# Kernel tuning notes

Hardware: AMD Instinct MI355X
Metric: run time of the kernel (lower is better)

## Reference

```python
import jax, jax.numpy as jnp
import numpy as np

N_NODES = 100000


def _graph_conv_right(feat, src, dst, W, b, n_nodes):
    # DGL GraphConv(norm='right'): since in_feats > out_feats, apply weight first,
    # then sum-aggregate messages over edges, divide by in-degree (clamped >= 1),
    # add bias, then relu activation.
    h = feat @ W                                   # [N, out]
    msg = jnp.take(h, src, axis=0)                 # [E, out] gather from source nodes
    agg = jax.ops.segment_sum(msg, dst, num_segments=n_nodes)  # [N, out]
    deg = jax.ops.segment_sum(jnp.ones_like(dst, dtype=feat.dtype), dst,
                              num_segments=n_nodes)
    deg = jnp.clip(deg, 1.0, None)                 # allow_zero_in_degree
    out = agg / deg[:, None] + b
    return jax.nn.relu(out)


def setup_inputs() -> dict:
    key = jax.random.key(0)
    ks = jax.random.split(key, 6)
    n_edges = 3200000
    in_dim, hidden_dim, out_dim = 128, 32, 12
    features = jax.random.normal(ks[0], (N_NODES, in_dim), dtype=jnp.float32)
    src = jax.random.randint(ks[1], (n_edges,), 0, N_NODES, dtype=jnp.int64 if jax.config.jax_enable_x64 else jnp.int32)
    dst = jax.random.randint(ks[2], (n_edges,), 0, N_NODES, dtype=jnp.int64 if jax.config.jax_enable_x64 else jnp.int32)
    W1 = jax.random.normal(ks[3], (in_dim, hidden_dim), dtype=jnp.float32) * (1.0 / np.sqrt(in_dim))
    b1 = jnp.zeros((hidden_dim,), dtype=jnp.float32)
    W2 = jax.random.normal(ks[4], (hidden_dim, out_dim), dtype=jnp.float32) * (1.0 / np.sqrt(hidden_dim))
    b2 = jnp.zeros((out_dim,), dtype=jnp.float32)
    return {"features": features, "src": src, "dst": dst,
            "W1": W1, "b1": b1, "W2": W2, "b2": b2}


def reference(features, src, dst, W1, b1, W2, b2):
    x = _graph_conv_right(features, src, dst, W1, b1, N_NODES)
    x = jax.nn.relu(x)  # extra F.relu after layer1 (idempotent, kept for fidelity)
    x = _graph_conv_right(x, src, dst, W2, b2, N_NODES)
    return x
```

## Files before the change

kernel.cpp:

```cpp
#include <hip/hip_runtime.h>
#include <hip/hip_fp16.h>

#define N_IN   128
#define HID    32
#define ODIM   12
#define RNODES 128
#define NBMAX  800
#define NBK2   1024
#define BCAP   4608
#define CHUNK  4096

__global__ __launch_bounds__(256) void gemm1_kernel(const float* __restrict__ feat,
                                                    const float* __restrict__ W1,
                                                    __half* __restrict__ h1, int nNodes) {
    __shared__ float sF[64 * 132];
    __shared__ float sW[N_IN * HID];
    const int tid = threadIdx.x;
    const int nb  = blockIdx.x * 64;

    {
        const float4* Wv  = (const float4*)W1;
        float4*       sWv = (float4*)sW;
        #pragma unroll
        for (int i = 0; i < 4; ++i) sWv[tid + 256 * i] = Wv[tid + 256 * i];
    }
    #pragma unroll
    for (int i = 0; i < 8; ++i) {
        int f   = tid + 256 * i;
        int row = f >> 5;
        int c4  = f & 31;
        int n   = nb + row;
        float4 v = make_float4(0.f, 0.f, 0.f, 0.f);
        if (n < nNodes) v = *(const float4*)(feat + (size_t)n * N_IN + c4 * 4);
        *(float4*)(sF + row * 132 + c4 * 4) = v;
    }
    __syncthreads();

    const int og = tid & 7;
    const int ng = tid >> 3;
    const int o0 = og * 4;
    const float* f0 = sF + ng * 132;
    const float* f1 = sF + (ng + 32) * 132;

    float acc0[4] = {0.f, 0.f, 0.f, 0.f};
    float acc1[4] = {0.f, 0.f, 0.f, 0.f};
    #pragma unroll 8
    for (int k = 0; k < N_IN; k += 4) {
        float4 a0 = *(const float4*)(f0 + k);
        float4 a1 = *(const float4*)(f1 + k);
        const float a0v[4] = {a0.x, a0.y, a0.z, a0.w};
        const float a1v[4] = {a1.x, a1.y, a1.z, a1.w};
        #pragma unroll
        for (int j = 0; j < 4; ++j) {
            float4 w = *(const float4*)(sW + (k + j) * HID + o0);
            acc0[0] += a0v[j] * w.x; acc0[1] += a0v[j] * w.y;
            acc0[2] += a0v[j] * w.z; acc0[3] += a0v[j] * w.w;
            acc1[0] += a1v[j] * w.x; acc1[1] += a1v[j] * w.y;
            acc1[2] += a1v[j] * w.z; acc1[3] += a1v[j] * w.w;
        }
    }
    int n0 = nb + ng, n1 = nb + ng + 32;
    if (n0 < nNodes) {
        union { __half2 h[2]; float2 f; } u;
        u.h[0] = __floats2half2_rn(acc0[0], acc0[1]);
        u.h[1] = __floats2half2_rn(acc0[2], acc0[3]);
        *(float2*)(h1 + (size_t)n0 * HID + o0) = u.f;
    }
    if (n1 < nNodes) {
        union { __half2 h[2]; float2 f; } u;
        u.h[0] = __floats2half2_rn(acc1[0], acc1[1]);
        u.h[1] = __floats2half2_rn(acc1[2], acc1[3]);
        *(float2*)(h1 + (size_t)n1 * HID + o0) = u.f;
    }
}

__global__ __launch_bounds__(512) void bplace_kernel(const int* __restrict__ src,
                                                     const int* __restrict__ dst,
                                                     int* __restrict__ bcur,
                                                     int* __restrict__ pairs, int nEdges) {
    __shared__ int      lh[NBK2];
    __shared__ int      lcur[NBK2];
    __shared__ int      gofs[NBK2];
    __shared__ int      sAux[512];
    __shared__ int      lst[CHUNK];
    __shared__ unsigned short lbk[CHUNK];

    const int tid  = threadIdx.x;
    const int base = blockIdx.x * CHUNK;
    const int m    = min(CHUNK, nEdges - base);

    lh[tid] = 0; lh[tid + 512] = 0;
    __syncthreads();

    int4 dv[2], sv[2];
    bool ok[2];
    #pragma unroll
    for (int k = 0; k < 2; ++k) {
        int e = base + k * 2048 + tid * 4;
        ok[k] = (e < nEdges);
        if (ok[k]) {
            dv[k] = *(const int4*)(dst + e);
            sv[k] = *(const int4*)(src + e);
        }
    }
    #pragma unroll
    for (int k = 0; k < 2; ++k) {
        if (ok[k]) {
            atomicAdd(&lh[dv[k].x >> 7], 1);
            atomicAdd(&lh[dv[k].y >> 7], 1);
            atomicAdd(&lh[dv[k].z >> 7], 1);
            atomicAdd(&lh[dv[k].w >> 7], 1);
        }
    }
    __syncthreads();

    int c0 = lh[2 * tid], c1 = lh[2 * tid + 1];
    int tsum = c0 + c1;
    sAux[tid] = tsum;
    __syncthreads();
    int inc = tsum;
    for (int off = 1; off < 512; off <<= 1) {
        int t = (tid >= off) ? sAux[tid - off] : 0;
        __syncthreads();
        inc += t;
        sAux[tid] = inc;
        __syncthreads();
    }
    int excl = inc - tsum;
    lh[2 * tid]     = excl;
    lh[2 * tid + 1] = excl + c0;
    lcur[2 * tid]     = excl;
    lcur[2 * tid + 1] = excl + c0;
    gofs[2 * tid]     = (c0 > 0) ? atomicAdd(&bcur[2 * tid], c0) : 0;
    gofs[2 * tid + 1] = (c1 > 0) ? atomicAdd(&bcur[2 * tid + 1], c1) : 0;
    __syncthreads();

    #pragma unroll
    for (int k = 0; k < 2; ++k) {
        if (ok[k]) {
            int b, p;
            b = dv[k].x >> 7; p = atomicAdd(&lcur[b], 1); lst[p] = ((dv[k].x & 127) << 17) | sv[k].x; lbk[p] = (unsigned short)b;
            b = dv[k].y >> 7; p = atomicAdd(&lcur[b], 1); lst[p] = ((dv[k].y & 127) << 17) | sv[k].y; lbk[p] = (unsigned short)b;
            b = dv[k].z >> 7; p = atomicAdd(&lcur[b], 1); lst[p] = ((dv[k].z & 127) << 17) | sv[k].z; lbk[p] = (unsigned short)b;
            b = dv[k].w >> 7; p = atomicAdd(&lcur[b], 1); lst[p] = ((dv[k].w & 127) << 17) | sv[k].w; lbk[p] = (unsigned short)b;
        }
    }
    __syncthreads();

    for (int i = tid; i < m; i += 512) {
        int b = lbk[i];
        int cap = gofs[b] + (i - lh[b]);
        if (cap < (b + 1) * BCAP - (b * BCAP) + 0) {}
        int rank = gofs[b] + (i - lh[b]);
        if (rank < BCAP) pairs[(size_t)b * BCAP + rank] = lst[i];
    }
}

__global__ __launch_bounds__(512) void agg1_kernel(const __half* __restrict__ h1,
                                                   const int* __restrict__ bcur,
                                                   const int* __restrict__ pairs,
                                                   const float* __restrict__ b1,
                                                   const float* __restrict__ W2,
                                                   __half* __restrict__ h2,
                                                   float* __restrict__ rdeg, int nNodes) {
    __shared__ int   sorted[BCAP];
    __shared__ int   hist[RNODES];
    __shared__ int   scn[RNODES];
    __shared__ int   cur[RNODES];
    __shared__ float sW2[HID * ODIM];
    const int tid = threadIdx.x;
    const int bkt = blockIdx.x;
    const int cnt = min(bcur[bkt], BCAP);
    const size_t pb = (size_t)bkt * BCAP;

    if (tid < RNODES) hist[tid] = 0;
    if (tid < 96) ((float4*)sW2)[tid] = ((const float4*)W2)[tid];
    __syncthreads();

    for (int i = tid; i < cnt; i += 512) atomicAdd(&hist[pairs[pb + i] >> 17], 1);
    __syncthreads();

    int v0 = (tid < RNODES) ? hist[tid] : 0;
    if (tid < RNODES) scn[tid] = v0;
    __syncthreads();
    int inc = v0;
    for (int off = 1; off < RNODES; off <<= 1) {
        int t = (tid < RNODES && tid >= off) ? scn[tid - off] : 0;
        __syncthreads();
        if (tid < RNODES) { inc += t; scn[tid] = inc; }
        __syncthreads();
    }
    if (tid < RNODES) { scn[tid] = inc - v0; cur[tid] = inc - v0; }
    __syncthreads();

    for (int i = tid; i < cnt; i += 512) {
        int v = pairs[pb + i];
        int pos = atomicAdd(&cur[v >> 17], 1);
        sorted[pos] = v & 0x1FFFF;
    }
    __syncthreads();

    const int c   = tid & 15;
    const int grp = tid >> 4;
    const __half2* h1v = (const __half2*)h1;
    const int col = (c < ODIM) ? c : 0;

    #pragma unroll
    for (int g = 0; g < 4; ++g) {
        int nl = g * 32 + grp;
        int n  = bkt * RNODES + nl;
        if (n >= nNodes) continue;
        int dcnt = hist[nl];
        int beg  = scn[nl];
        int end  = beg + dcnt;

        float2 s0 = {0.f, 0.f}, s1 = {0.f, 0.f}, s2 = {0.f, 0.f}, s3 = {0.f, 0.f};
        int i = beg;
        for (; i + 4 <= end; i += 4) {
            int e0 = sorted[i], e1 = sorted[i + 1], e2 = sorted[i + 2], e3 = sorted[i + 3];
            float2 f0 = __half22float2(h1v[(size_t)e0 * 16 + c]);
            float2 f1 = __half22float2(h1v[(size_t)e1 * 16 + c]);
            float2 f2 = __half22float2(h1v[(size_t)e2 * 16 + c]);
            float2 f3 = __half22float2(h1v[(size_t)e3 * 16 + c]);
            s0.x += f0.x; s0.y += f0.y;
            s1.x += f1.x; s1.y += f1.y;
            s2.x += f2.x; s2.y += f2.y;
            s3.x += f3.x; s3.y += f3.y;
        }
        for (; i < end; ++i) {
            float2 f = __half22float2(h1v[(size_t)sorted[i] * 16 + c]);
            s0.x += f.x; s0.y += f.y;
        }
        float sumx = (s0.x + s1.x) + (s2.x + s3.x);
        float sumy = (s0.y + s1.y) + (s2.y + s3.y);

        float rd = 1.f / (float)(dcnt < 1 ? 1 : dcnt);
        float x0 = sumx * rd + b1[2 * c];
        float x1 = sumy * rd + b1[2 * c + 1];
        x0 = x0 > 0.f ? x0 : 0.f;
        x1 = x1 > 0.f ? x1 : 0.f;

        float acc = 0.f;
        #pragma unroll
        for (int k = 0; k < 16; ++k) {
            float xk0 = __shfl(x0, k, 16);
            float xk1 = __shfl(x1, k, 16);
            acc += xk0 * sW2[(2 * k) * ODIM + col] + xk1 * sW2[(2 * k + 1) * ODIM + col];
        }
        if (c < ODIM) h2[(size_t)n * ODIM + c] = __float2half(acc);
        if (c == 0)   rdeg[n] = rd;
    }
}

__global__ __launch_bounds__(512) void agg2_kernel(const __half* __restrict__ h2,
                                                   const int* __restrict__ bcur,
                                                   const int* __restrict__ pairs,
                                                   const float* __restrict__ rdeg,
                                                   const float* __restrict__ b2,
                                                   float* __restrict__ out, int nNodes) {
    __shared__ int sorted[BCAP];
    __shared__ int hist[RNODES];
    __shared__ int scn[RNODES];
    __shared__ int cur[RNODES];
    const int tid = threadIdx.x;
    const int bkt = blockIdx.x;
    const int cnt = min(bcur[bkt], BCAP);
    const size_t pb = (size_t)bkt * BCAP;

    if (tid < RNODES) hist[tid] = 0;
    __syncthreads();

    for (int i = tid; i < cnt; i += 512) atomicAdd(&hist[pairs[pb + i] >> 17], 1);
    __syncthreads();

    int v0 = (tid < RNODES) ? hist[tid] : 0;
    if (tid < RNODES) scn[tid] = v0;
    __syncthreads();
    int inc = v0;
    for (int off = 1; off < RNODES; off <<= 1) {
        int t = (tid < RNODES && tid >= off) ? scn[tid - off] : 0;
        __syncthreads();
        if (tid < RNODES) { inc += t; scn[tid] = inc; }
        __syncthreads();
    }
    if (tid < RNODES) { scn[tid] = inc - v0; cur[tid] = inc - v0; }
    __syncthreads();

    for (int i = tid; i < cnt; i += 512) {
        int v = pairs[pb + i];
        int pos = atomicAdd(&cur[v >> 17], 1);
        sorted[pos] = v & 0x1FFFF;
    }
    __syncthreads();

    const int c   = tid & 7;
    const int grp = tid >> 3;
    const int cc  = (c < 6) ? c : 0;
    const __half2* h2v = (const __half2*)h2;

    #pragma unroll
    for (int g = 0; g < 2; ++g) {
        int nl = g * 64 + grp;
        int n  = bkt * RNODES + nl;
        if (n >= nNodes) continue;
        int dcnt = hist[nl];
        int beg  = scn[nl];
        int end  = beg + dcnt;

        float2 s0 = {0.f, 0.f}, s1 = {0.f, 0.f}, s2 = {0.f, 0.f}, s3 = {0.f, 0.f};
        int i = beg;
        for (; i + 4 <= end; i += 4) {
            int e0 = sorted[i], e1 = sorted[i + 1], e2 = sorted[i + 2], e3 = sorted[i + 3];
            float2 f0 = __half22float2(h2v[(size_t)e0 * 6 + cc]);
            float2 f1 = __half22float2(h2v[(size_t)e1 * 6 + cc]);
            float2 f2 = __half22float2(h2v[(size_t)e2 * 6 + cc]);
            float2 f3 = __half22float2(h2v[(size_t)e3 * 6 + cc]);
            s0.x += f0.x; s0.y += f0.y;
            s1.x += f1.x; s1.y += f1.y;
            s2.x += f2.x; s2.y += f2.y;
            s3.x += f3.x; s3.y += f3.y;
        }
        for (; i < end; ++i) {
            float2 f = __half22float2(h2v[(size_t)sorted[i] * 6 + cc]);
            s0.x += f.x; s0.y += f.y;
        }
        float sumx = (s0.x + s1.x) + (s2.x + s3.x);
        float sumy = (s0.y + s1.y) + (s2.y + s3.y);

        float rd = rdeg[n];
        float w0 = sumx * rd + b2[2 * cc];
        float w1 = sumy * rd + b2[2 * cc + 1];
        w0 = w0 > 0.f ? w0 : 0.f;
        w1 = w1 > 0.f ? w1 : 0.f;
        if (c < 6) *(float2*)(out + (size_t)n * ODIM + 2 * c) = make_float2(w0, w1);
    }
}

extern "C" void kernel_launch(void* const* d_in, const int* in_sizes, int n_in,
                              void* d_out, int out_size, void* d_ws, size_t ws_size,
                              hipStream_t stream) {
    const float* feat = (const float*)d_in[0];
    const int*   src  = (const int*)d_in[1];
    const int*   dst  = (const int*)d_in[2];
    const float* W1   = (const float*)d_in[3];
    const float* b1   = (const float*)d_in[4];
    const float* W2   = (const float*)d_in[5];
    const float* b2   = (const float*)d_in[6];
    float* out = (float*)d_out;

    const int nEdges = in_sizes[1];
    const int nNodes = in_sizes[0] / N_IN;
    const int nb     = (nNodes + RNODES - 1) / RNODES;

    __half* h1   = (__half*)d_ws;
    __half* h2   = h1 + (size_t)nNodes * HID;
    float*  rdeg = (float*)(h2 + (size_t)nNodes * ODIM);
    int*    bcur = (int*)(rdeg + nNodes);
    int*    pairs = bcur + NBK2;

    hipMemsetAsync(bcur, 0, NBK2 * sizeof(int), stream);

    gemm1_kernel<<<(nNodes + 63) / 64, 256, 0, stream>>>(feat, W1, h1, nNodes);
    bplace_kernel<<<(nEdges + CHUNK - 1) / CHUNK, 512, 0, stream>>>(src, dst, bcur, pairs, nEdges);
    agg1_kernel<<<nb, 512, 0, stream>>>(h1, bcur, pairs, b1, W2, h2, rdeg, nNodes);
    agg2_kernel<<<nb, 512, 0, stream>>>(h2, bcur, pairs, rdeg, b2, out, nNodes);
}
```

Before: 238.9 us.

## Persist CSR from agg1 and simplify agg2 to direct row-range gathers

agg1 now writes its per-bucket sorted source indices back into the pairs buffer, along with a global row start and count for each node. agg2 no longer repeats the histogram, prefix scan and scatter sort; it reads this CSR directly with one 8-thread group per node in smaller 256-thread blocks. Both gather loops are also unrolled to 8 edges to keep more loads in flight. The cost is an extra global write of about 3.2M indices plus two per-node arrays in agg1, and agg2 reads the indices from global memory instead of LDS.

```diff
diff --git a/kernel.cpp b/kernel.cpp
--- a/kernel.cpp
+++ b/kernel.cpp
@@ -127,8 +127,8 @@
         __syncthreads();
     }
     int excl = inc - tsum;
-    lh[2 * tid]     = excl;
-    lh[2 * tid + 1] = excl + c0;
+    lh[2 * tid]       = excl;
+    lh[2 * tid + 1]   = excl + c0;
     lcur[2 * tid]     = excl;
     lcur[2 * tid + 1] = excl + c0;
     gofs[2 * tid]     = (c0 > 0) ? atomicAdd(&bcur[2 * tid], c0) : 0;
@@ -149,8 +149,6 @@
 
     for (int i = tid; i < m; i += 512) {
         int b = lbk[i];
-        int cap = gofs[b] + (i - lh[b]);
-        if (cap < (b + 1) * BCAP - (b * BCAP) + 0) {}
         int rank = gofs[b] + (i - lh[b]);
         if (rank < BCAP) pairs[(size_t)b * BCAP + rank] = lst[i];
     }
@@ -158,11 +156,13 @@
 
 __global__ __launch_bounds__(512) void agg1_kernel(const __half* __restrict__ h1,
                                                    const int* __restrict__ bcur,
-                                                   const int* __restrict__ pairs,
+                                                   int* __restrict__ pairs,
                                                    const float* __restrict__ b1,
                                                    const float* __restrict__ W2,
                                                    __half* __restrict__ h2,
-                                                   float* __restrict__ rdeg, int nNodes) {
+                                                   float* __restrict__ rdeg,
+                                                   int* __restrict__ rowstartg,
+                                                   int* __restrict__ countg, int nNodes) {
     __shared__ int   sorted[BCAP];
     __shared__ int   hist[RNODES];
     __shared__ int   scn[RNODES];
@@ -200,6 +200,15 @@
     }
     __syncthreads();
 
+    for (int i = tid; i < cnt; i += 512) pairs[pb + i] = sorted[i];
+    if (tid < RNODES) {
+        int n = bkt * RNODES + tid;
+        if (n < nNodes) {
+            rowstartg[n] = (int)pb + scn[tid];
+            countg[n]    = hist[tid];
+        }
+    }
+
     const int c   = tid & 15;
     const int grp = tid >> 4;
     const __half2* h1v = (const __half2*)h1;
@@ -216,16 +225,30 @@
 
         float2 s0 = {0.f, 0.f}, s1 = {0.f, 0.f}, s2 = {0.f, 0.f}, s3 = {0.f, 0.f};
         int i = beg;
+        for (; i + 8 <= end; i += 8) {
+            int e0 = sorted[i],     e1 = sorted[i + 1], e2 = sorted[i + 2], e3 = sorted[i + 3];
+            int e4 = sorted[i + 4], e5 = sorted[i + 5], e6 = sorted[i + 6], e7 = sorted[i + 7];
+            float2 f0 = __half22float2(h1v[(size_t)e0 * 16 + c]);
+            float2 f1 = __half22float2(h1v[(size_t)e1 * 16 + c]);
+            float2 f2 = __half22float2(h1v[(size_t)e2 * 16 + c]);
+            float2 f3 = __half22float2(h1v[(size_t)e3 * 16 + c]);
+            float2 f4 = __half22float2(h1v[(size_t)e4 * 16 + c]);
+            float2 f5 = __half22float2(h1v[(size_t)e5 * 16 + c]);
+            float2 f6 = __half22float2(h1v[(size_t)e6 * 16 + c]);
+            float2 f7 = __half22float2(h1v[(size_t)e7 * 16 + c]);
+            s0.x += f0.x; s0.y += f0.y;  s1.x += f1.x; s1.y += f1.y;
+            s2.x += f2.x; s2.y += f2.y;  s3.x += f3.x; s3.y += f3.y;
+            s0.x += f4.x; s0.y += f4.y;  s1.x += f5.x; s1.y += f5.y;
+            s2.x += f6.x; s2.y += f6.y;  s3.x += f7.x; s3.y += f7.y;
+        }
         for (; i + 4 <= end; i += 4) {
             int e0 = sorted[i], e1 = sorted[i + 1], e2 = sorted[i + 2], e3 = sorted[i + 3];
             float2 f0 = __half22float2(h1v[(size_t)e0 * 16 + c]);
             float2 f1 = __half22float2(h1v[(size_t)e1 * 16 + c]);
             float2 f2 = __half22float2(h1v[(size_t)e2 * 16 + c]);
             float2 f3 = __half22float2(h1v[(size_t)e3 * 16 + c]);
-            s0.x += f0.x; s0.y += f0.y;
-            s1.x += f1.x; s1.y += f1.y;
-            s2.x += f2.x; s2.y += f2.y;
-            s3.x += f3.x; s3.y += f3.y;
+            s0.x += f0.x; s0.y += f0.y;  s1.x += f1.x; s1.y += f1.y;
+            s2.x += f2.x; s2.y += f2.y;  s3.x += f3.x; s3.y += f3.y;
         }
         for (; i < end; ++i) {
             float2 f = __half22float2(h1v[(size_t)sorted[i] * 16 + c]);
@@ -252,88 +275,64 @@
     }
 }
 
-__global__ __launch_bounds__(512) void agg2_kernel(const __half* __restrict__ h2,
-                                                   const int* __restrict__ bcur,
-                                                   const int* __restrict__ pairs,
+__global__ __launch_bounds__(256) void agg2_kernel(const __half* __restrict__ h2,
+                                                   const int* __restrict__ rowstartg,
+                                                   const int* __restrict__ countg,
+                                                   const int* __restrict__ eidx,
                                                    const float* __restrict__ rdeg,
                                                    const float* __restrict__ b2,
                                                    float* __restrict__ out, int nNodes) {
-    __shared__ int sorted[BCAP];
-    __shared__ int hist[RNODES];
-    __shared__ int scn[RNODES];
-    __shared__ int cur[RNODES];
     const int tid = threadIdx.x;
-    const int bkt = blockIdx.x;
-    const int cnt = min(bcur[bkt], BCAP);
-    const size_t pb = (size_t)bkt * BCAP;
-
-    if (tid < RNODES) hist[tid] = 0;
-    __syncthreads();
-
-    for (int i = tid; i < cnt; i += 512) atomicAdd(&hist[pairs[pb + i] >> 17], 1);
-    __syncthreads();
-
-    int v0 = (tid < RNODES) ? hist[tid] : 0;
-    if (tid < RNODES) scn[tid] = v0;
-    __syncthreads();
-    int inc = v0;
-    for (int off = 1; off < RNODES; off <<= 1) {
-        int t = (tid < RNODES && tid >= off) ? scn[tid - off] : 0;
-        __syncthreads();
-        if (tid < RNODES) { inc += t; scn[tid] = inc; }
-        __syncthreads();
-    }
-    if (tid < RNODES) { scn[tid] = inc - v0; cur[tid] = inc - v0; }
-    __syncthreads();
-
-    for (int i = tid; i < cnt; i += 512) {
-        int v = pairs[pb + i];
-        int pos = atomicAdd(&cur[v >> 17], 1);
-        sorted[pos] = v & 0x1FFFF;
-    }
-    __syncthreads();
-
-    const int c   = tid & 7;
-    const int grp = tid >> 3;
+    const int n = blockIdx.x * 32 + (tid >> 3);
+    const int c = tid & 7;
+    if (n >= nNodes) return;
+
+    const int cnt = countg[n];
+    const int beg = rowstartg[n];
+    const int end = beg + cnt;
     const int cc  = (c < 6) ? c : 0;
     const __half2* h2v = (const __half2*)h2;
 
-    #pragma unroll
-    for (int g = 0; g < 2; ++g) {
-        int nl = g * 64 + grp;
-        int n  = bkt * RNODES + nl;
-        if (n >= nNodes) continue;
-        int dcnt = hist[nl];
-        int beg  = scn[nl];
-        int end  = beg + dcnt;
-
-        float2 s0 = {0.f, 0.f}, s1 = {0.f, 0.f}, s2 = {0.f, 0.f}, s3 = {0.f, 0.f};
-        int i = beg;
-        for (; i + 4 <= end; i += 4) {
-            int e0 = sorted[i], e1 = sorted[i + 1], e2 = sorted[i + 2], e3 = sorted[i + 3];
-            float2 f0 = __half22float2(h2v[(size_t)e0 * 6 + cc]);
-            float2 f1 = __half22float2(h2v[(size_t)e1 * 6 + cc]);
-            float2 f2 = __half22float2(h2v[(size_t)e2 * 6 + cc]);
-            float2 f3 = __half22float2(h2v[(size_t)e3 * 6 + cc]);
-            s0.x += f0.x; s0.y += f0.y;
-            s1.x += f1.x; s1.y += f1.y;
-            s2.x += f2.x; s2.y += f2.y;
-            s3.x += f3.x; s3.y += f3.y;
-        }
-        for (; i < end; ++i) {
-            float2 f = __half22float2(h2v[(size_t)sorted[i] * 6 + cc]);
-            s0.x += f.x; s0.y += f.y;
-        }
-        float sumx = (s0.x + s1.x) + (s2.x + s3.x);
-        float sumy = (s0.y + s1.y) + (s2.y + s3.y);
-
-        float rd = rdeg[n];
-        float w0 = sumx * rd + b2[2 * cc];
-        float w1 = sumy * rd + b2[2 * cc + 1];
-        w0 = w0 > 0.f ? w0 : 0.f;
-        w1 = w1 > 0.f ? w1 : 0.f;
-        if (c < 6) *(float2*)(out + (size_t)n * ODIM + 2 * c) = make_float2(w0, w1);
-    }
+    float2 s0 = {0.f, 0.f}, s1 = {0.f, 0.f}, s2 = {0.f, 0.f}, s3 = {0.f, 0.f};
+    int i = beg;
+    for (; i + 8 <= end; i += 8) {
+        int e0 = eidx[i],     e1 = eidx[i + 1], e2 = eidx[i + 2], e3 = eidx[i + 3];
+        int e4 = eidx[i + 4], e5 = eidx[i + 5], e6 = eidx[i + 6], e7 = eidx[i + 7];
+        float2 f0 = __half22float2(h2v[(size_t)e0 * 6 + cc]);
+        float2 f1 = __half22float2(h2v[(size_t)e1 * 6 + cc]);
+        float2 f2 = __half22float2(h2v[(size_t)e2 * 6 + cc]);
+        float2 f3 = __half22float2(h2v[(size_t)e3 * 6 + cc]);
+        float2 f4 = __half22float2(h2v[(size_t)e4 * 6 + cc]);
+        float2 f5 = __half22float2(h2v[(size_t)e5 * 6 + cc]);
+        float2 f6 = __half22float2(h2v[(size_t)e6 * 6 + cc]);
+        float2 f7 = __half22float2(h2v[(size_t)e7 * 6 + cc]);
+        s0.x += f0.x; s0.y += f0.y;  s1.x += f1.x; s1.y += f1.y;
+        s2.x += f2.x; s2.y += f2.y;  s3.x += f3.x; s3.y += f3.y;
+        s0.x += f4.x; s0.y += f4.y;  s1.x += f5.x; s1.y += f5.y;
+        s2.x += f6.x; s2.y += f6.y;  s3.x += f7.x; s3.y += f7.y;
+    }
+    for (; i + 4 <= end; i += 4) {
+        int e0 = eidx[i], e1 = eidx[i + 1], e2 = eidx[i + 2], e3 = eidx[i + 3];
+        float2 f0 = __half22float2(h2v[(size_t)e0 * 6 + cc]);
+        float2 f1 = __half22float2(h2v[(size_t)e1 * 6 + cc]);
+        float2 f2 = __half22float2(h2v[(size_t)e2 * 6 + cc]);
+        float2 f3 = __half22float2(h2v[(size_t)e3 * 6 + cc]);
+        s0.x += f0.x; s0.y += f0.y;  s1.x += f1.x; s1.y += f1.y;
+        s2.x += f2.x; s2.y += f2.y;  s3.x += f3.x; s3.y += f3.y;
+    }
+    for (; i < end; ++i) {
+        float2 f = __half22float2(h2v[(size_t)eidx[i] * 6 + cc]);
+        s0.x += f.x; s0.y += f.y;
+    }
+    float sumx = (s0.x + s1.x) + (s2.x + s3.x);
+    float sumy = (s0.y + s1.y) + (s2.y + s3.y);
+
+    float rd = rdeg[n];
+    float w0 = sumx * rd + b2[2 * cc];
+    float w1 = sumy * rd + b2[2 * cc + 1];
+    w0 = w0 > 0.f ? w0 : 0.f;
+    w1 = w1 > 0.f ? w1 : 0.f;
+    if (c < 6) *(float2*)(out + (size_t)n * ODIM + 2 * c) = make_float2(w0, w1);
 }
 
 extern "C" void kernel_launch(void* const* d_in, const int* in_sizes, int n_in,
@@ -352,16 +351,18 @@
     const int nNodes = in_sizes[0] / N_IN;
     const int nb     = (nNodes + RNODES - 1) / RNODES;
 
-    __half* h1   = (__half*)d_ws;
-    __half* h2   = h1 + (size_t)nNodes * HID;
-    float*  rdeg = (float*)(h2 + (size_t)nNodes * ODIM);
-    int*    bcur = (int*)(rdeg + nNodes);
-    int*    pairs = bcur + NBK2;
+    __half* h1       = (__half*)d_ws;
+    __half* h2       = h1 + (size_t)nNodes * HID;
+    float*  rdeg     = (float*)(h2 + (size_t)nNodes * ODIM);
+    int*    rowstart = (int*)(rdeg + nNodes);
+    int*    countg   = rowstart + nNodes;
+    int*    bcur     = countg + nNodes;
+    int*    pairs    = bcur + NBK2;
 
     hipMemsetAsync(bcur, 0, NBK2 * sizeof(int), stream);
 
     gemm1_kernel<<<(nNodes + 63) / 64, 256, 0, stream>>>(feat, W1, h1, nNodes);
     bplace_kernel<<<(nEdges + CHUNK - 1) / CHUNK, 512, 0, stream>>>(src, dst, bcur, pairs, nEdges);
-    agg1_kernel<<<nb, 512, 0, stream>>>(h1, bcur, pairs, b1, W2, h2, rdeg, nNodes);
-    agg2_kernel<<<nb, 512, 0, stream>>>(h2, bcur, pairs, rdeg, b2, out, nNodes);
-}
+    agg1_kernel<<<nb, 512, 0, stream>>>(h1, bcur, pairs, b1, W2, h2, rdeg, rowstart, countg, nNodes);
+    agg2_kernel<<<(nNodes + 31) / 32, 256, 0, stream>>>(h2, rowstart, countg, pairs, rdeg, b2, out, nNodes);
+}
```

Result: no change. 235.5 us (-1.5%).
